# Performance work log

Measured on AMD Instinct MI355X. Metric: run time of the kernel, lower is better.

## Reference

```python
import jax, jax.numpy as jnp
import numpy as np

B, S, D, E, K = 4, 4096, 2048, 64, 2
LN_EPS = 1e-5
TEMP_EPS = 1e-6
Z_LOSS_COEF = 0.001
LB_COEF = 0.1


def setup_inputs() -> dict:
    key = jax.random.key(0)
    k1, k2 = jax.random.split(key)
    x = jax.random.normal(k1, (B, S, D), dtype=jnp.float32)
    # kaiming_normal fan_in (std = 1/sqrt(D)) scaled by 0.01, as in __init__
    W = jax.random.normal(k2, (E, D), dtype=jnp.float32) * jnp.float32(0.01 / np.sqrt(D))
    gamma = jnp.ones((E,), jnp.float32)   # LayerNorm weight
    beta = jnp.zeros((E,), jnp.float32)   # LayerNorm bias
    temperature = jnp.full((1,), 0.5, jnp.float32)
    return {"x": x, "W": W, "gamma": gamma, "beta": beta, "temperature": temperature}


def reference(x, W, gamma, beta, temperature):
    b, s, d = x.shape
    xf = x.reshape(-1, d)                                  # [N, D]
    logits = xf @ W.T                                      # [N, E]
    # LayerNorm over expert dim (biased variance, eps=1e-5, matches torch)
    mu = logits.mean(axis=-1, keepdims=True)
    var = jnp.mean(jnp.square(logits - mu), axis=-1, keepdims=True)
    logits = (logits - mu) * jax.lax.rsqrt(var + LN_EPS) * gamma + beta
    # temperature-scaled softmax
    routing_weights = jax.nn.softmax(logits / (temperature + TEMP_EPS), axis=-1)  # [N, E]
    # top-k + scatter into dense dispatch mask
    top_w, top_idx = jax.lax.top_k(routing_weights, K)     # [N, K]
    n = routing_weights.shape[0]
    dispatch = jnp.zeros_like(routing_weights).at[jnp.arange(n)[:, None], top_idx].set(top_w)
    dispatch = dispatch.reshape(b, s, E)                   # [B, S, E]
    # aux losses
    expert_load = dispatch.mean(axis=1)                    # [B, E]
    load_balance_loss = jnp.std(expert_load, ddof=1) / expert_load.mean() * 10.0
    router_z_loss = jnp.mean(jnp.square(logits))
    total_loss = ZLC * router_z_loss + LB_COEF * load_balance_loss if False else (
        Z_LOSS_COEF * router_z_loss + LB_COEF * load_balance_loss)
    return jax.lax.stop_gradient(routing_weights), dispatch, total_loss
```

## Files before the change

### kernel.cpp

```cpp
#include <hip/hip_runtime.h>
#include <hip/hip_bf16.h>
#include <float.h>
#include <math.h>

#define B_DIM 4
#define S_DIM 4096
#define D_DIM 2048
#define E_DIM 64
#define N_TOK 16384
#define TOKS 32
#define NBLK (N_TOK / TOKS)
#define NTHR 128
#define BK 64
#define LDK 72
#define KSTEPS (D_DIM / BK)
#define GAP_THRESH 1e-3f
#define MAXFLAG 16

typedef __bf16 bf16x8_t __attribute__((ext_vector_type(8)));
typedef float f32x4_t __attribute__((ext_vector_type(4)));

union U8 { bf16x8_t v; unsigned short u[8]; };

__device__ __forceinline__ void split2(float f, unsigned short& h, unsigned short& l) {
    unsigned int u = __float_as_uint(f);
    h = (unsigned short)(u >> 16);
    float hf = __uint_as_float(u & 0xFFFF0000u);
    l = (unsigned short)(__float_as_uint(f - hf) >> 16);
}

__global__ __launch_bounds__(NTHR, 2) void router_main(
    const float* __restrict__ x, const float* __restrict__ W,
    const float* __restrict__ gamma, const float* __restrict__ beta,
    const float* __restrict__ temperature,
    float* __restrict__ out_rw, float* __restrict__ out_dp,
    float* __restrict__ g_zsum, float* __restrict__ g_load)
{
    __shared__ unsigned short wh[2][E_DIM][LDK];
    __shared__ unsigned short wl[2][E_DIM][LDK];
    __shared__ float lgt[TOKS][E_DIM + 1];
    __shared__ float lgm[E_DIM], lbt[E_DIM], loadsum[E_DIM];
    __shared__ float smu[TOKS], srs[TOKS], sinv[TOKS];
    __shared__ int sel1[TOKS], sel2[TOKS];
    __shared__ int ftok[MAXFLAG], fcand[MAXFLAG][3];
    __shared__ int nflag;

    const int tid = threadIdx.x;
    const int tokBase = blockIdx.x * TOKS;
    const int lane = tid & 63;
    const int wv = tid >> 6;
    const int l15 = lane & 15;
    const int quad = lane >> 4;

    if (tid == 0) nflag = 0;
    if (tid < E_DIM) { lgm[tid] = gamma[tid]; lbt[tid] = beta[tid]; loadsum[tid] = 0.f; }

    const int rowW = tid >> 1;
    const int colW = (tid & 1) * 32;
    const float* wp = W + (size_t)rowW * D_DIM + colW;

    const float* xp = x + (size_t)(tokBase + wv * 16 + l15) * D_DIM + quad * 8;

    f32x4_t acc[4];
    #pragma unroll
    for (int t = 0; t < 4; ++t) acc[t] = (f32x4_t){0.f, 0.f, 0.f, 0.f};

    float4 wreg[8], xq[4], xn[4];
    #pragma unroll
    for (int j = 0; j < 8; ++j) wreg[j] = *(const float4*)(wp + j * 4);
    #pragma unroll
    for (int c = 0; c < 2; ++c) {
        xq[c * 2]     = *(const float4*)(xp + c * 32);
        xq[c * 2 + 1] = *(const float4*)(xp + c * 32 + 4);
    }
    #pragma unroll
    for (int j = 0; j < 8; ++j) {
        ushort4 h, l;
        split2(wreg[j].x, h.x, l.x); split2(wreg[j].y, h.y, l.y);
        split2(wreg[j].z, h.z, l.z); split2(wreg[j].w, h.w, l.w);
        *(ushort4*)&wh[0][rowW][colW + j * 4] = h;
        *(ushort4*)&wl[0][rowW][colW + j * 4] = l;
    }
    __syncthreads();

    for (int s = 0; s < KSTEPS; ++s) {
        const int cur = s & 1;
        const bool more = (s + 1 < KSTEPS);
        if (more) {
            const float* wq = wp + (s + 1) * BK;
            #pragma unroll
            for (int j = 0; j < 8; ++j) wreg[j] = *(const float4*)(wq + j * 4);
            const float* xg = xp + (s + 1) * BK;
            #pragma unroll
            for (int c = 0; c < 2; ++c) {
                xn[c * 2]     = *(const float4*)(xg + c * 32);
                xn[c * 2 + 1] = *(const float4*)(xg + c * 32 + 4);
            }
        }
        #pragma unroll
        for (int h = 0; h < 2; ++h) {
            float tf[8] = {xq[h*2].x, xq[h*2].y, xq[h*2].z, xq[h*2].w,
                           xq[h*2+1].x, xq[h*2+1].y, xq[h*2+1].z, xq[h*2+1].w};
            U8 ah, al;
            #pragma unroll
            for (int k = 0; k < 8; ++k) split2(tf[k], ah.u[k], al.u[k]);
            #pragma unroll
            for (int t = 0; t < 4; ++t) {
                U8 bh, bl;
                bh.v = *(const bf16x8_t*)&wh[cur][t * 16 + l15][h * 32 + quad * 8];
                bl.v = *(const bf16x8_t*)&wl[cur][t * 16 + l15][h * 32 + quad * 8];
                acc[t] = __builtin_amdgcn_mfma_f32_16x16x32_bf16(ah.v, bh.v, acc[t], 0, 0, 0);
                acc[t] = __builtin_amdgcn_mfma_f32_16x16x32_bf16(ah.v, bl.v, acc[t], 0, 0, 0);
                acc[t] = __builtin_amdgcn_mfma_f32_16x16x32_bf16(al.v, bh.v, acc[t], 0, 0, 0);
            }
        }
        if (more) {
            const int nxt = cur ^ 1;
            #pragma unroll
            for (int j = 0; j < 8; ++j) {
                ushort4 h, l;
                split2(wreg[j].x, h.x, l.x); split2(wreg[j].y, h.y, l.y);
                split2(wreg[j].z, h.z, l.z); split2(wreg[j].w, h.w, l.w);
                *(ushort4*)&wh[nxt][rowW][colW + j * 4] = h;
                *(ushort4*)&wl[nxt][rowW][colW + j * 4] = l;
            }
            #pragma unroll
            for (int j = 0; j < 4; ++j) xq[j] = xn[j];
        }
        __syncthreads();
    }

    #pragma unroll
    for (int t = 0; t < 4; ++t)
        #pragma unroll
        for (int r = 0; r < 4; ++r)
            lgt[wv * 16 + quad * 4 + r][t * 16 + l15] = acc[t][r];
    __syncthreads();

    const int tok = wv * 16 + l15;
    const int q = quad;
    const float it = 1.f / (temperature[0] + 1e-6f);
    float s1 = 0.f, s2 = 0.f;
    #pragma unroll
    for (int e = 0; e < 16; ++e) { float v = lgt[tok][q * 16 + e]; s1 += v; s2 += v * v; }
    s1 += __shfl_xor(s1, 16); s1 += __shfl_xor(s1, 32);
    s2 += __shfl_xor(s2, 16); s2 += __shfl_xor(s2, 32);
    const float mu  = s1 * (1.f / 64.f);
    const float var = s2 * (1.f / 64.f) - mu * mu;
    const float rs  = rsqrtf(var + 1e-5f);
    if (q == 0) { smu[tok] = mu; srs[tok] = rs; }

    float m0 = -FLT_MAX, m1 = -FLT_MAX, m2 = -FLT_MAX;
    int   i0 = -1, i1 = -1, i2 = -1;
    float zl = 0.f;
    #pragma unroll
    for (int e = 0; e < 16; ++e) {
        int c = q * 16 + e;
        float y = (lgt[tok][c] - mu) * rs * lgm[c] + lbt[c];
        lgt[tok][c] = y;
        zl += y * y;
        if (y > m0)      { m2 = m1; i2 = i1; m1 = m0; i1 = i0; m0 = y; i0 = c; }
        else if (y > m1) { m2 = m1; i2 = i1; m1 = y; i1 = c; }
        else if (y > m2) { m2 = y; i2 = c; }
    }
    #pragma unroll
    for (int d = 16; d <= 32; d <<= 1) {
        float n0 = __shfl_xor(m0, d), n1 = __shfl_xor(m1, d), n2 = __shfl_xor(m2, d);
        int   j0 = __shfl_xor(i0, d), j1 = __shfl_xor(i1, d), j2 = __shfl_xor(i2, d);
        bool t0 = (m0 > n0) || (m0 == n0 && i0 < j0);
        float r0v = t0 ? m0 : n0; int r0i = t0 ? i0 : j0;
        float A0v = t0 ? m1 : m0; int A0i = t0 ? i1 : i0;
        float A1v = t0 ? m2 : m1; int A1i = t0 ? i2 : i1;
        float B0v = t0 ? n0 : n1; int B0i = t0 ? j0 : j1;
        float B1v = t0 ? n1 : n2; int B1i = t0 ? j1 : j2;
        bool t1 = (A0v > B0v) || (A0v == B0v && A0i < B0i);
        float r1v = t1 ? A0v : B0v; int r1i = t1 ? A0i : B0i;
        float A0w = t1 ? A1v : A0v; int A0j = t1 ? A1i : A0i;
        float B0w = t1 ? B0v : B1v; int B0j = t1 ? B0i : B1i;
        bool t2 = (A0w > B0w) || (A0w == B0w && A0j < B0j);
        float r2v = t2 ? A0w : B0w; int r2i = t2 ? A0j : B0j;
        m0 = r0v; i0 = r0i; m1 = r1v; i1 = r1i; m2 = r2v; i2 = r2i;
    }
    if (q == 0) {
        sel1[tok] = i0; sel2[tok] = i1;
        if (m1 - m2 < GAP_THRESH) {
            int sf = atomicAdd(&nflag, 1);
            if (sf < MAXFLAG) { ftok[sf] = tok; fcand[sf][0] = i0; fcand[sf][1] = i1; fcand[sf][2] = i2; }
        }
    }
    float es = 0.f;
    #pragma unroll
    for (int e = 0; e < 16; ++e) {
        int c = q * 16 + e;
        float ev = __expf((lgt[tok][c] - m0) * it);
        lgt[tok][c] = ev; es += ev;
    }
    es += __shfl_xor(es, 16); es += __shfl_xor(es, 32);
    if (q == 0) sinv[tok] = 1.f / es;
    zl += __shfl_xor(zl, 1); zl += __shfl_xor(zl, 2); zl += __shfl_xor(zl, 4);
    zl += __shfl_xor(zl, 8); zl += __shfl_xor(zl, 16); zl += __shfl_xor(zl, 32);
    if (lane == 0) atomicAdd(g_zsum, zl);
    __syncthreads();

    const int nf = min(nflag, MAXFLAG);
    for (int f = wv; f < nf; f += 2) {
        const int tk = ftok[f];
        const int c0 = fcand[f][0], c1 = fcand[f][1], c2 = fcand[f][2];
        const float* xr = x + (size_t)(tokBase + tk) * D_DIM;
        const float* w0 = W + (size_t)c0 * D_DIM;
        const float* w1 = W + (size_t)c1 * D_DIM;
        const float* w2 = W + (size_t)c2 * D_DIM;
        double L0 = 0.0, L1 = 0.0, L2 = 0.0;
        for (int i = lane; i < D_DIM; i += 64) {
            double xv = (double)xr[i];
            L0 += xv * (double)w0[i];
            L1 += xv * (double)w1[i];
            L2 += xv * (double)w2[i];
        }
        #pragma unroll
        for (int off = 32; off; off >>= 1) {
            L0 += __shfl_down(L0, off);
            L1 += __shfl_down(L1, off);
            L2 += __shfl_down(L2, off);
        }
        if (lane == 0) {
            double dmu = (double)smu[tk], drs = (double)srs[tk];
            double y0 = (L0 - dmu) * drs * (double)lgm[c0] + (double)lbt[c0];
            double y1 = (L1 - dmu) * drs * (double)lgm[c1] + (double)lbt[c1];
            double y2 = (L2 - dmu) * drs * (double)lgm[c2] + (double)lbt[c2];
            bool g01 = (y0 > y1) || (y0 == y1 && c0 < c1);
            bool g02 = (y0 > y2) || (y0 == y2 && c0 < c2);
            bool g12 = (y1 > y2) || (y1 == y2 && c1 < c2);
            int a, b;
            if (!g01 && !g02)      { a = c1; b = c2; }
            else if (g01 && !g12)  { a = c0; b = c2; }
            else                   { a = c0; b = c1; }
            sel1[tk] = a; sel2[tk] = b;
        }
    }
    __syncthreads();

    if (tid < TOKS) {
        float inv = sinv[tid];
        atomicAdd(&loadsum[sel1[tid]], lgt[tid][sel1[tid]] * inv);
        atomicAdd(&loadsum[sel2[tid]], lgt[tid][sel2[tid]] * inv);
    }
    __syncthreads();
    if (tid < E_DIM) atomicAdd(&g_load[(tokBase >> 12) * E_DIM + tid], loadsum[tid]);

    float* orw = out_rw + (size_t)tokBase * E_DIM;
    float* odp = out_dp + (size_t)tokBase * E_DIM;
    for (int i = tid; i < TOKS * E_DIM; i += NTHR) {
        int r = i >> 6, c = i & 63;
        float p = lgt[r][c] * sinv[r];
        orw[i] = p;
        odp[i] = (c == sel1[r] || c == sel2[r]) ? p : 0.f;
    }
}

__global__ void router_fin(const float* __restrict__ ws, float* __restrict__ out_loss) {
    __shared__ float sv[B_DIM * E_DIM];
    const int tid = threadIdx.x;
    sv[tid] = ws[8 + tid] * (1.f / S_DIM);
    __syncthreads();
    if (tid == 0) {
        float s = 0.f;
        for (int i = 0; i < B_DIM * E_DIM; ++i) s += sv[i];
        const float mean = s * (1.f / (B_DIM * E_DIM));
        float ss = 0.f;
        for (int i = 0; i < B_DIM * E_DIM; ++i) { float d = sv[i] - mean; ss += d * d; }
        const float sd = sqrtf(ss * (1.f / (B_DIM * E_DIM - 1)));
        const float z = ws[0] * (1.f / ((float)N_TOK * E_DIM));
        out_loss[0] = 0.001f * z + 0.1f * (sd / mean) * 10.f;
    }
}

extern "C" void kernel_launch(void* const* d_in, const int* in_sizes, int n_in,
                              void* d_out, int out_size, void* d_ws, size_t ws_size,
                              hipStream_t stream) {
    const float* x     = (const float*)d_in[0];
    const float* W     = (const float*)d_in[1];
    const float* gamma = (const float*)d_in[2];
    const float* beta  = (const float*)d_in[3];
    const float* temp  = (const float*)d_in[4];
    float* out  = (float*)d_out;
    float* rw   = out;
    float* dp   = out + (size_t)N_TOK * E_DIM;
    float* loss = out + 2 * (size_t)N_TOK * E_DIM;
    float* ws   = (float*)d_ws;

    hipMemsetAsync(d_ws, 0, 512 * sizeof(float), stream);
    router_main<<<dim3(NBLK), dim3(NTHR), 0, stream>>>(x, W, gamma, beta, temp,
                                                       rw, dp, ws, ws + 8);
    router_fin<<<dim3(1), dim3(256), 0, stream>>>(ws, loss);
}
```

Before: 262.2 us.

## Split-K router GEMM with precomputed bf16 weight halves and separate epilogue kernel

Moves the W hi/lo bf16 split into a one-time conversion kernel, so the main GEMM reads pre-split weights straight from global memory (L2-resident) instead of staging and splitting them in LDS every K step. The GEMM is split four ways along K, with more tokens per block, and partial logits go to a workspace buffer, or are accumulated atomically into the output when the workspace is small. A new wave-per-token epilogue kernel reduces the partials, then applies LayerNorm, top-k with the fp64 tie fallback, softmax and the load/z reductions, using sharded atomic slots. This adds a fourth kernel launch and extra global traffic for the partials in exchange for more parallelism and no LDS staging in the GEMM.

After: 270.5 us. 3.2% more time.

```diff
diff --git a/kernel.cpp b/kernel.cpp
--- a/kernel.cpp
+++ b/kernel.cpp
@@ -8,18 +8,24 @@
 #define D_DIM 2048
 #define E_DIM 64
 #define N_TOK 16384
-#define TOKS 32
-#define NBLK (N_TOK / TOKS)
-#define NTHR 128
-#define BK 64
-#define LDK 72
-#define KSTEPS (D_DIM / BK)
+#define SPLITK 4
+#define KSLICE (D_DIM / SPLITK)
+#define MSTEP (KSLICE / 32)
+#define TPB 128
+#define NMAIN ((N_TOK / TPB) * SPLITK)
+#define EPB 16
+#define NEPI (N_TOK / EPB)
 #define GAP_THRESH 1e-3f
-#define MAXFLAG 16
+
+#define WS_WLO_B   262144
+#define WS_HEAD_B  524288
+#define WS_PART_B  540672
+#define WS_NEED    (WS_PART_B + (size_t)SPLITK * N_TOK * E_DIM * 4)
+#define HEAD_ZSLOT 0
+#define HEAD_LOADP 64
 
 typedef __bf16 bf16x8_t __attribute__((ext_vector_type(8)));
 typedef float f32x4_t __attribute__((ext_vector_type(4)));
-
 union U8 { bf16x8_t v; unsigned short u[8]; };
 
 __device__ __forceinline__ void split2(float f, unsigned short& h, unsigned short& l) {
@@ -29,249 +35,218 @@
     l = (unsigned short)(__float_as_uint(f - hf) >> 16);
 }
 
-__global__ __launch_bounds__(NTHR, 2) void router_main(
-    const float* __restrict__ x, const float* __restrict__ W,
-    const float* __restrict__ gamma, const float* __restrict__ beta,
-    const float* __restrict__ temperature,
+__global__ __launch_bounds__(256) void wconv(const float* __restrict__ W,
+                                             unsigned short* __restrict__ whi,
+                                             unsigned short* __restrict__ wlo) {
+    const int t = blockIdx.x * 256 + threadIdx.x;
+    float4 v = *(const float4*)(W + (size_t)t * 4);
+    ushort4 h, l;
+    split2(v.x, h.x, l.x); split2(v.y, h.y, l.y);
+    split2(v.z, h.z, l.z); split2(v.w, h.w, l.w);
+    *(ushort4*)(whi + (size_t)t * 4) = h;
+    *(ushort4*)(wlo + (size_t)t * 4) = l;
+}
+
+template<bool ATOMIC>
+__global__ __launch_bounds__(256, 2) void router_main(
+    const float* __restrict__ x,
+    const unsigned short* __restrict__ whi, const unsigned short* __restrict__ wlo,
+    float* __restrict__ part)
+{
+    const int tid = threadIdx.x;
+    const int lane = tid & 63, wv = tid >> 6;
+    const int l15 = lane & 15, quad = lane >> 4;
+    const int slice = blockIdx.x & (SPLITK - 1);
+    const int grp = blockIdx.x >> 2;
+    const int tokBase = grp * TPB + wv * 32;
+    const int k0 = slice * KSLICE;
+
+    const float* xb[2];
+    xb[0] = x + (size_t)(tokBase + l15) * D_DIM + k0 + quad * 8;
+    xb[1] = x + (size_t)(tokBase + 16 + l15) * D_DIM + k0 + quad * 8;
+
+    f32x4_t acc[2][4];
+    #pragma unroll
+    for (int m = 0; m < 2; ++m)
+        #pragma unroll
+        for (int t = 0; t < 4; ++t) acc[m][t] = (f32x4_t){0.f, 0.f, 0.f, 0.f};
+
+    float4 xq[2][2], xn[2][2];
+    #pragma unroll
+    for (int m = 0; m < 2; ++m) {
+        xq[m][0] = *(const float4*)(xb[m]);
+        xq[m][1] = *(const float4*)(xb[m] + 4);
+    }
+
+    #pragma unroll 4
+    for (int s = 0; s < MSTEP; ++s) {
+        if (s + 1 < MSTEP) {
+            #pragma unroll
+            for (int m = 0; m < 2; ++m) {
+                const float* p = xb[m] + (s + 1) * 32;
+                xn[m][0] = *(const float4*)(p);
+                xn[m][1] = *(const float4*)(p + 4);
+            }
+        }
+        const int kk = k0 + s * 32 + quad * 8;
+        bf16x8_t bh[4], bl[4];
+        #pragma unroll
+        for (int t = 0; t < 4; ++t) {
+            const size_t off = (size_t)(t * 16 + l15) * D_DIM + kk;
+            bh[t] = *(const bf16x8_t*)(whi + off);
+            bl[t] = *(const bf16x8_t*)(wlo + off);
+        }
+        #pragma unroll
+        for (int m = 0; m < 2; ++m) {
+            float tf[8] = {xq[m][0].x, xq[m][0].y, xq[m][0].z, xq[m][0].w,
+                           xq[m][1].x, xq[m][1].y, xq[m][1].z, xq[m][1].w};
+            U8 ah, al;
+            #pragma unroll
+            for (int k = 0; k < 8; ++k) split2(tf[k], ah.u[k], al.u[k]);
+            #pragma unroll
+            for (int t = 0; t < 4; ++t) {
+                acc[m][t] = __builtin_amdgcn_mfma_f32_16x16x32_bf16(ah.v, bh[t], acc[m][t], 0, 0, 0);
+                acc[m][t] = __builtin_amdgcn_mfma_f32_16x16x32_bf16(ah.v, bl[t], acc[m][t], 0, 0, 0);
+                acc[m][t] = __builtin_amdgcn_mfma_f32_16x16x32_bf16(al.v, bh[t], acc[m][t], 0, 0, 0);
+            }
+        }
+        if (s + 1 < MSTEP) {
+            #pragma unroll
+            for (int m = 0; m < 2; ++m) { xq[m][0] = xn[m][0]; xq[m][1] = xn[m][1]; }
+        }
+    }
+
+    #pragma unroll
+    for (int m = 0; m < 2; ++m)
+        #pragma unroll
+        for (int t = 0; t < 4; ++t)
+            #pragma unroll
+            for (int r = 0; r < 4; ++r) {
+                const int token = tokBase + m * 16 + quad * 4 + r;
+                const int e = t * 16 + l15;
+                if (ATOMIC) atomicAdd(&part[(size_t)token * E_DIM + e], acc[m][t][r]);
+                else part[((size_t)slice * N_TOK + token) * E_DIM + e] = acc[m][t][r];
+            }
+}
+
+__device__ __forceinline__ void wave_argmax(float y, float& mv, int& mi) {
+    float v = y; int ix = threadIdx.x & 63;
+    #pragma unroll
+    for (int d = 32; d; d >>= 1) {
+        float ov = __shfl_xor(v, d); int oi = __shfl_xor(ix, d);
+        if (ov > v || (ov == v && oi < ix)) { v = ov; ix = oi; }
+    }
+    mv = v; mi = ix;
+}
+
+template<bool ATOMIC>
+__global__ __launch_bounds__(1024) void router_epi(
+    const float* __restrict__ part, const float* __restrict__ x,
+    const float* __restrict__ W, const float* __restrict__ gamma,
+    const float* __restrict__ beta, const float* __restrict__ temperature,
     float* __restrict__ out_rw, float* __restrict__ out_dp,
-    float* __restrict__ g_zsum, float* __restrict__ g_load)
+    float* __restrict__ zslot, float* __restrict__ loadp)
 {
-    __shared__ unsigned short wh[2][E_DIM][LDK];
-    __shared__ unsigned short wl[2][E_DIM][LDK];
-    __shared__ float lgt[TOKS][E_DIM + 1];
-    __shared__ float lgm[E_DIM], lbt[E_DIM], loadsum[E_DIM];
-    __shared__ float smu[TOKS], srs[TOKS], sinv[TOKS];
-    __shared__ int sel1[TOKS], sel2[TOKS];
-    __shared__ int ftok[MAXFLAG], fcand[MAXFLAG][3];
-    __shared__ int nflag;
-
+    __shared__ float loadsum[E_DIM];
+    __shared__ float zred[EPB];
     const int tid = threadIdx.x;
-    const int tokBase = blockIdx.x * TOKS;
-    const int lane = tid & 63;
-    const int wv = tid >> 6;
-    const int l15 = lane & 15;
-    const int quad = lane >> 4;
-
-    if (tid == 0) nflag = 0;
-    if (tid < E_DIM) { lgm[tid] = gamma[tid]; lbt[tid] = beta[tid]; loadsum[tid] = 0.f; }
-
-    const int rowW = tid >> 1;
-    const int colW = (tid & 1) * 32;
-    const float* wp = W + (size_t)rowW * D_DIM + colW;
-
-    const float* xp = x + (size_t)(tokBase + wv * 16 + l15) * D_DIM + quad * 8;
-
-    f32x4_t acc[4];
-    #pragma unroll
-    for (int t = 0; t < 4; ++t) acc[t] = (f32x4_t){0.f, 0.f, 0.f, 0.f};
-
-    float4 wreg[8], xq[4], xn[4];
-    #pragma unroll
-    for (int j = 0; j < 8; ++j) wreg[j] = *(const float4*)(wp + j * 4);
-    #pragma unroll
-    for (int c = 0; c < 2; ++c) {
-        xq[c * 2]     = *(const float4*)(xp + c * 32);
-        xq[c * 2 + 1] = *(const float4*)(xp + c * 32 + 4);
-    }
-    #pragma unroll
-    for (int j = 0; j < 8; ++j) {
-        ushort4 h, l;
-        split2(wreg[j].x, h.x, l.x); split2(wreg[j].y, h.y, l.y);
-        split2(wreg[j].z, h.z, l.z); split2(wreg[j].w, h.w, l.w);
-        *(ushort4*)&wh[0][rowW][colW + j * 4] = h;
-        *(ushort4*)&wl[0][rowW][colW + j * 4] = l;
-    }
+    const int lane = tid & 63, wv = tid >> 6;
+    const int tok = blockIdx.x * EPB + wv;
+    if (tid < E_DIM) loadsum[tid] = 0.f;
     __syncthreads();
 
-    for (int s = 0; s < KSTEPS; ++s) {
-        const int cur = s & 1;
-        const bool more = (s + 1 < KSTEPS);
-        if (more) {
-            const float* wq = wp + (s + 1) * BK;
-            #pragma unroll
-            for (int j = 0; j < 8; ++j) wreg[j] = *(const float4*)(wq + j * 4);
-            const float* xg = xp + (s + 1) * BK;
-            #pragma unroll
-            for (int c = 0; c < 2; ++c) {
-                xn[c * 2]     = *(const float4*)(xg + c * 32);
-                xn[c * 2 + 1] = *(const float4*)(xg + c * 32 + 4);
-            }
-        }
-        #pragma unroll
-        for (int h = 0; h < 2; ++h) {
-            float tf[8] = {xq[h*2].x, xq[h*2].y, xq[h*2].z, xq[h*2].w,
-                           xq[h*2+1].x, xq[h*2+1].y, xq[h*2+1].z, xq[h*2+1].w};
-            U8 ah, al;
-            #pragma unroll
-            for (int k = 0; k < 8; ++k) split2(tf[k], ah.u[k], al.u[k]);
-            #pragma unroll
-            for (int t = 0; t < 4; ++t) {
-                U8 bh, bl;
-                bh.v = *(const bf16x8_t*)&wh[cur][t * 16 + l15][h * 32 + quad * 8];
-                bl.v = *(const bf16x8_t*)&wl[cur][t * 16 + l15][h * 32 + quad * 8];
-                acc[t] = __builtin_amdgcn_mfma_f32_16x16x32_bf16(ah.v, bh.v, acc[t], 0, 0, 0);
-                acc[t] = __builtin_amdgcn_mfma_f32_16x16x32_bf16(ah.v, bl.v, acc[t], 0, 0, 0);
-                acc[t] = __builtin_amdgcn_mfma_f32_16x16x32_bf16(al.v, bh.v, acc[t], 0, 0, 0);
-            }
-        }
-        if (more) {
-            const int nxt = cur ^ 1;
-            #pragma unroll
-            for (int j = 0; j < 8; ++j) {
-                ushort4 h, l;
-                split2(wreg[j].x, h.x, l.x); split2(wreg[j].y, h.y, l.y);
-                split2(wreg[j].z, h.z, l.z); split2(wreg[j].w, h.w, l.w);
-                *(ushort4*)&wh[nxt][rowW][colW + j * 4] = h;
-                *(ushort4*)&wl[nxt][rowW][colW + j * 4] = l;
-            }
-            #pragma unroll
-            for (int j = 0; j < 4; ++j) xq[j] = xn[j];
-        }
-        __syncthreads();
-    }
-
-    #pragma unroll
-    for (int t = 0; t < 4; ++t)
-        #pragma unroll
-        for (int r = 0; r < 4; ++r)
-            lgt[wv * 16 + quad * 4 + r][t * 16 + l15] = acc[t][r];
+    float p;
+    if (ATOMIC) p = part[(size_t)tok * E_DIM + lane];
+    else {
+        p = 0.f;
+        #pragma unroll
+        for (int s = 0; s < SPLITK; ++s) p += part[((size_t)s * N_TOK + tok) * E_DIM + lane];
+    }
+    float s1 = p, s2 = p * p;
+    #pragma unroll
+    for (int d = 32; d; d >>= 1) { s1 += __shfl_xor(s1, d); s2 += __shfl_xor(s2, d); }
+    const float mu = s1 * (1.f / 64.f);
+    const float var = s2 * (1.f / 64.f) - mu * mu;
+    const float rs = rsqrtf(var + 1e-5f);
+    const float y = (p - mu) * rs * gamma[lane] + beta[lane];
+
+    float zl = y * y;
+    #pragma unroll
+    for (int d = 32; d; d >>= 1) zl += __shfl_xor(zl, d);
+    if (lane == 0) zred[wv] = zl;
+
+    float m0, m1, m2; int i0, i1, i2;
+    wave_argmax(y, m0, i0);
+    wave_argmax((lane == i0) ? -FLT_MAX : y, m1, i1);
+    wave_argmax((lane == i0 || lane == i1) ? -FLT_MAX : y, m2, i2);
+    int sa = i0, sb = i1;
+
+    if (m1 - m2 < GAP_THRESH) {
+        const float* xr = x + (size_t)tok * D_DIM;
+        const int c[3] = {i0, i1, i2};
+        double L[3];
+        #pragma unroll
+        for (int j = 0; j < 3; ++j) {
+            const float* wr = W + (size_t)c[j] * D_DIM;
+            double a = 0.0;
+            for (int i = lane; i < D_DIM; i += 64) a += (double)xr[i] * (double)wr[i];
+            #pragma unroll
+            for (int d = 32; d; d >>= 1) a += __shfl_xor(a, d);
+            L[j] = a;
+        }
+        double yy[3];
+        #pragma unroll
+        for (int j = 0; j < 3; ++j)
+            yy[j] = (L[j] - (double)mu) * (double)rs * (double)gamma[c[j]] + (double)beta[c[j]];
+        bool g01 = (yy[0] > yy[1]) || (yy[0] == yy[1] && c[0] < c[1]);
+        bool g02 = (yy[0] > yy[2]) || (yy[0] == yy[2] && c[0] < c[2]);
+        bool g12 = (yy[1] > yy[2]) || (yy[1] == yy[2] && c[1] < c[2]);
+        if (!g01 && !g02)     { sa = c[1]; sb = c[2]; }
+        else if (g01 && !g12) { sa = c[0]; sb = c[2]; }
+        else                  { sa = c[0]; sb = c[1]; }
+    }
+
+    const float it = 1.f / (temperature[0] + 1e-6f);
+    float ev = __expf((y - m0) * it);
+    float es = ev;
+    #pragma unroll
+    for (int d = 32; d; d >>= 1) es += __shfl_xor(es, d);
+    const float prob = ev / es;
+
+    out_rw[(size_t)tok * E_DIM + lane] = prob;
+    const bool sel = (lane == sa || lane == sb);
+    out_dp[(size_t)tok * E_DIM + lane] = sel ? prob : 0.f;
+    if (sel) atomicAdd(&loadsum[lane], prob);
     __syncthreads();
 
-    const int tok = wv * 16 + l15;
-    const int q = quad;
-    const float it = 1.f / (temperature[0] + 1e-6f);
-    float s1 = 0.f, s2 = 0.f;
-    #pragma unroll
-    for (int e = 0; e < 16; ++e) { float v = lgt[tok][q * 16 + e]; s1 += v; s2 += v * v; }
-    s1 += __shfl_xor(s1, 16); s1 += __shfl_xor(s1, 32);
-    s2 += __shfl_xor(s2, 16); s2 += __shfl_xor(s2, 32);
-    const float mu  = s1 * (1.f / 64.f);
-    const float var = s2 * (1.f / 64.f) - mu * mu;
-    const float rs  = rsqrtf(var + 1e-5f);
-    if (q == 0) { smu[tok] = mu; srs[tok] = rs; }
-
-    float m0 = -FLT_MAX, m1 = -FLT_MAX, m2 = -FLT_MAX;
-    int   i0 = -1, i1 = -1, i2 = -1;
-    float zl = 0.f;
-    #pragma unroll
-    for (int e = 0; e < 16; ++e) {
-        int c = q * 16 + e;
-        float y = (lgt[tok][c] - mu) * rs * lgm[c] + lbt[c];
-        lgt[tok][c] = y;
-        zl += y * y;
-        if (y > m0)      { m2 = m1; i2 = i1; m1 = m0; i1 = i0; m0 = y; i0 = c; }
-        else if (y > m1) { m2 = m1; i2 = i1; m1 = y; i1 = c; }
-        else if (y > m2) { m2 = y; i2 = c; }
-    }
-    #pragma unroll
-    for (int d = 16; d <= 32; d <<= 1) {
-        float n0 = __shfl_xor(m0, d), n1 = __shfl_xor(m1, d), n2 = __shfl_xor(m2, d);
-        int   j0 = __shfl_xor(i0, d), j1 = __shfl_xor(i1, d), j2 = __shfl_xor(i2, d);
-        bool t0 = (m0 > n0) || (m0 == n0 && i0 < j0);
-        float r0v = t0 ? m0 : n0; int r0i = t0 ? i0 : j0;
-        float A0v = t0 ? m1 : m0; int A0i = t0 ? i1 : i0;
-        float A1v = t0 ? m2 : m1; int A1i = t0 ? i2 : i1;
-        float B0v = t0 ? n0 : n1; int B0i = t0 ? j0 : j1;
-        float B1v = t0 ? n1 : n2; int B1i = t0 ? j1 : j2;
-        bool t1 = (A0v > B0v) || (A0v == B0v && A0i < B0i);
-        float r1v = t1 ? A0v : B0v; int r1i = t1 ? A0i : B0i;
-        float A0w = t1 ? A1v : A0v; int A0j = t1 ? A1i : A0i;
-        float B0w = t1 ? B0v : B1v; int B0j = t1 ? B0i : B1i;
-        bool t2 = (A0w > B0w) || (A0w == B0w && A0j < B0j);
-        float r2v = t2 ? A0w : B0w; int r2i = t2 ? A0j : B0j;
-        m0 = r0v; i0 = r0i; m1 = r1v; i1 = r1i; m2 = r2v; i2 = r2i;
-    }
-    if (q == 0) {
-        sel1[tok] = i0; sel2[tok] = i1;
-        if (m1 - m2 < GAP_THRESH) {
-            int sf = atomicAdd(&nflag, 1);
-            if (sf < MAXFLAG) { ftok[sf] = tok; fcand[sf][0] = i0; fcand[sf][1] = i1; fcand[sf][2] = i2; }
-        }
-    }
-    float es = 0.f;
-    #pragma unroll
-    for (int e = 0; e < 16; ++e) {
-        int c = q * 16 + e;
-        float ev = __expf((lgt[tok][c] - m0) * it);
-        lgt[tok][c] = ev; es += ev;
-    }
-    es += __shfl_xor(es, 16); es += __shfl_xor(es, 32);
-    if (q == 0) sinv[tok] = 1.f / es;
-    zl += __shfl_xor(zl, 1); zl += __shfl_xor(zl, 2); zl += __shfl_xor(zl, 4);
-    zl += __shfl_xor(zl, 8); zl += __shfl_xor(zl, 16); zl += __shfl_xor(zl, 32);
-    if (lane == 0) atomicAdd(g_zsum, zl);
-    __syncthreads();
-
-    const int nf = min(nflag, MAXFLAG);
-    for (int f = wv; f < nf; f += 2) {
-        const int tk = ftok[f];
-        const int c0 = fcand[f][0], c1 = fcand[f][1], c2 = fcand[f][2];
-        const float* xr = x + (size_t)(tokBase + tk) * D_DIM;
-        const float* w0 = W + (size_t)c0 * D_DIM;
-        const float* w1 = W + (size_t)c1 * D_DIM;
-        const float* w2 = W + (size_t)c2 * D_DIM;
-        double L0 = 0.0, L1 = 0.0, L2 = 0.0;
-        for (int i = lane; i < D_DIM; i += 64) {
-            double xv = (double)xr[i];
-            L0 += xv * (double)w0[i];
-            L1 += xv * (double)w1[i];
-            L2 += xv * (double)w2[i];
-        }
-        #pragma unroll
-        for (int off = 32; off; off >>= 1) {
-            L0 += __shfl_down(L0, off);
-            L1 += __shfl_down(L1, off);
-            L2 += __shfl_down(L2, off);
-        }
-        if (lane == 0) {
-            double dmu = (double)smu[tk], drs = (double)srs[tk];
-            double y0 = (L0 - dmu) * drs * (double)lgm[c0] + (double)lbt[c0];
-            double y1 = (L1 - dmu) * drs * (double)lgm[c1] + (double)lbt[c1];
-            double y2 = (L2 - dmu) * drs * (double)lgm[c2] + (double)lbt[c2];
-            bool g01 = (y0 > y1) || (y0 == y1 && c0 < c1);
-            bool g02 = (y0 > y2) || (y0 == y2 && c0 < c2);
-            bool g12 = (y1 > y2) || (y1 == y2 && c1 < c2);
-            int a, b;
-            if (!g01 && !g02)      { a = c1; b = c2; }
-            else if (g01 && !g12)  { a = c0; b = c2; }
-            else                   { a = c0; b = c1; }
-            sel1[tk] = a; sel2[tk] = b;
-        }
-    }
-    __syncthreads();
-
-    if (tid < TOKS) {
-        float inv = sinv[tid];
-        atomicAdd(&loadsum[sel1[tid]], lgt[tid][sel1[tid]] * inv);
-        atomicAdd(&loadsum[sel2[tid]], lgt[tid][sel2[tid]] * inv);
-    }
-    __syncthreads();
-    if (tid < E_DIM) atomicAdd(&g_load[(tokBase >> 12) * E_DIM + tid], loadsum[tid]);
-
-    float* orw = out_rw + (size_t)tokBase * E_DIM;
-    float* odp = out_dp + (size_t)tokBase * E_DIM;
-    for (int i = tid; i < TOKS * E_DIM; i += NTHR) {
-        int r = i >> 6, c = i & 63;
-        float p = lgt[r][c] * sinv[r];
-        orw[i] = p;
-        odp[i] = (c == sel1[r] || c == sel2[r]) ? p : 0.f;
-    }
-}
-
-__global__ void router_fin(const float* __restrict__ ws, float* __restrict__ out_loss) {
+    if (tid == 0) {
+        float z = 0.f;
+        #pragma unroll
+        for (int i = 0; i < EPB; ++i) z += zred[i];
+        atomicAdd(&zslot[blockIdx.x & 63], z);
+    }
+    const int b = (blockIdx.x * EPB) >> 12;
+    if (tid < E_DIM) atomicAdd(&loadp[(blockIdx.x & 7) * 256 + b * E_DIM + tid], loadsum[tid]);
+}
+
+__global__ void router_fin(const float* __restrict__ head, float* __restrict__ out_loss) {
     __shared__ float sv[B_DIM * E_DIM];
     const int tid = threadIdx.x;
-    sv[tid] = ws[8 + tid] * (1.f / S_DIM);
+    float s = 0.f;
+    #pragma unroll
+    for (int pl = 0; pl < 8; ++pl) s += head[HEAD_LOADP + pl * 256 + tid];
+    sv[tid] = s * (1.f / S_DIM);
     __syncthreads();
     if (tid == 0) {
-        float s = 0.f;
-        for (int i = 0; i < B_DIM * E_DIM; ++i) s += sv[i];
-        const float mean = s * (1.f / (B_DIM * E_DIM));
+        float t = 0.f;
+        for (int i = 0; i < B_DIM * E_DIM; ++i) t += sv[i];
+        const float mean = t * (1.f / (B_DIM * E_DIM));
         float ss = 0.f;
         for (int i = 0; i < B_DIM * E_DIM; ++i) { float d = sv[i] - mean; ss += d * d; }
         const float sd = sqrtf(ss * (1.f / (B_DIM * E_DIM - 1)));
-        const float z = ws[0] * (1.f / ((float)N_TOK * E_DIM));
-        out_loss[0] = 0.001f * z + 0.1f * (sd / mean) * 10.f;
+        float z = 0.f;
+        for (int i = 0; i < 64; ++i) z += head[HEAD_ZSLOT + i];
+        out_loss[0] = 0.001f * (z * (1.f / ((float)N_TOK * E_DIM))) + 0.1f * (sd / mean) * 10.f;
     }
 }
 
@@ -287,10 +262,26 @@
     float* rw   = out;
     float* dp   = out + (size_t)N_TOK * E_DIM;
     float* loss = out + 2 * (size_t)N_TOK * E_DIM;
-    float* ws   = (float*)d_ws;
-
-    hipMemsetAsync(d_ws, 0, 512 * sizeof(float), stream);
-    router_main<<<dim3(NBLK), dim3(NTHR), 0, stream>>>(x, W, gamma, beta, temp,
-                                                       rw, dp, ws, ws + 8);
-    router_fin<<<dim3(1), dim3(256), 0, stream>>>(ws, loss);
-}
+
+    unsigned short* whi = (unsigned short*)d_ws;
+    unsigned short* wlo = (unsigned short*)((char*)d_ws + WS_WLO_B);
+    float* head = (float*)((char*)d_ws + WS_HEAD_B);
+    float* partbuf = (float*)((char*)d_ws + WS_PART_B);
+    const bool store_path = (ws_size >= WS_NEED);
+
+    hipMemsetAsync((char*)d_ws + WS_HEAD_B, 0, 16384, stream);
+    wconv<<<dim3(128), dim3(256), 0, stream>>>(W, whi, wlo);
+    if (store_path) {
+        router_main<false><<<dim3(NMAIN), dim3(256), 0, stream>>>(x, whi, wlo, partbuf);
+        router_epi<false><<<dim3(NEPI), dim3(1024), 0, stream>>>(
+            partbuf, x, W, gamma, beta, temp, rw, dp,
+            head + HEAD_ZSLOT, head + HEAD_LOADP);
+    } else {
+        hipMemsetAsync(rw, 0, (size_t)N_TOK * E_DIM * 4, stream);
+        router_main<true><<<dim3(NMAIN), dim3(256), 0, stream>>>(x, whi, wlo, rw);
+        router_epi<true><<<dim3(NEPI), dim3(1024), 0, stream>>>(
+            rw, x, W, gamma, beta, temp, rw, dp,
+            head + HEAD_ZSLOT, head + HEAD_LOADP);
+    }
+    router_fin<<<dim3(1), dim3(256), 0, stream>>>(head, loss);
+}
```
